# Performance work log

Hardware: AMD Instinct MI355X
Metric: run time of the kernel (lower is better)

Reference implementation:

```python
import jax, jax.numpy as jnp
import numpy as np

DELTA = 0.0          # init kwarg (torch default is 0.7; 0.0 used so random data selects pairs)
N, T = 1_048_576, 32  # samples x trait columns
COS_EPS = 1e-8       # torch.cosine_similarity eps


def setup_inputs() -> dict:
    key = jax.random.key(0)
    k1, k2 = jax.random.split(key)
    return {
        "y_pred": jax.random.normal(k1, (N, T), dtype=jnp.float32),
        "y_true": jax.random.normal(k2, (N, T), dtype=jnp.float32),
    }


def reference(y_pred, y_true):
    t = y_true.shape[1]
    # Pearson correlation matrix over columns of y_true (centered Gram + norm outer)
    xc = y_true - jnp.mean(y_true, axis=0, keepdims=True)      # [N, T]
    nx = jnp.sqrt(jnp.sum(xc * xc, axis=0))                    # [T]
    pcc = jnp.einsum('nj,nk->jk', xc, xc) / (nx[:, None] * nx[None, :])
    # Cosine similarity matrix over columns of y_pred
    pn = jnp.sqrt(jnp.sum(y_pred * y_pred, axis=0))            # [T]
    denom = jnp.maximum(pn[:, None] * pn[None, :], COS_EPS)
    cos = jnp.einsum('nj,nk->jk', y_pred, y_pred) / denom      # [T, T]
    # Pair mask: 1 <= j < k < T (loop starts at j=1 in the original)
    idx = jnp.arange(t)
    pair_mask = (idx[None, :] > idx[:, None]) & (idx[:, None] >= 1)
    sel = pair_mask & (pcc >= DELTA)
    c = (t - 1) * (t - 2) // 2                                 # total pair count (incl. unselected)
    total = jnp.sum(jnp.where(sel, 1.0 - cos, 0.0))
    return total / c
```

## Files before the change

### kernel.cpp

```cpp
#include <hip/hip_runtime.h>

#define N_ROWS   1048576
#define T_COLS   32
#define NBLK     1024
#define BLOCK    256
#define ROWS_PER_WAVEPAIR 512
#define CHUNKS   (ROWS_PER_WAVEPAIR / 16)
#define NWS      2080

typedef _Float16 half8   __attribute__((ext_vector_type(8)));
typedef float    floatx16 __attribute__((ext_vector_type(16)));

__global__ __launch_bounds__(256, 4) void ts_gram(const float* __restrict__ y_pred,
                                                  const float* __restrict__ y_true,
                                                  float* __restrict__ ws) {
    __shared__ float s_red[NWS];

    const int tid  = threadIdx.x;
    const int wv   = tid >> 6;
    const int mtx  = wv >> 1;
    const int sub  = wv & 1;
    const int lane = tid & 63;
    const int half = lane >> 5;
    const int col  = lane & 31;

    const float* src = (mtx == 0) ? y_true : y_pred;
    const size_t row0 = ((size_t)blockIdx.x * 2 + sub) * ROWS_PER_WAVEPAIR;
    const float* p = src + row0 * T_COLS + (size_t)half * 8 * T_COLS + col;

    floatx16 acc = {};
    float lsum = 0.0f;

    #pragma unroll 2
    for (int c = 0; c < CHUNKS; ++c) {
        const float* cp = p + (size_t)c * 16 * T_COLS;
        float v[8];
        #pragma unroll
        for (int j = 0; j < 8; ++j) v[j] = cp[j * T_COLS];
        half8 h;
        #pragma unroll
        for (int j = 0; j < 8; ++j) h[j] = (_Float16)v[j];
        if (mtx == 0) {
            #pragma unroll
            for (int j = 0; j < 8; ++j) lsum += v[j];
        }
        acc = __builtin_amdgcn_mfma_f32_32x32x16_f16(h, h, acc, 0, 0, 0);
    }

    for (int i = tid; i < NWS; i += BLOCK) s_red[i] = 0.0f;
    __syncthreads();
    #pragma unroll
    for (int r = 0; r < 16; ++r) {
        int row = (r & 3) + 8 * (r >> 2) + 4 * half;
        atomicAdd(&s_red[mtx * 1024 + row * 32 + col], acc[r]);
    }
    if (mtx == 0) atomicAdd(&s_red[2048 + col], lsum);
    __syncthreads();
    for (int i = tid; i < NWS; i += BLOCK) atomicAdd(&ws[i], s_red[i]);
}

__global__ __launch_bounds__(1024) void ts_final(const float* __restrict__ w,
                                                 float* __restrict__ out) {
    __shared__ float s_S[32], s_nx[32], s_pn[32];
    __shared__ float s_red[16];
    const int tid = threadIdx.x;
    const float invN = 1.0f / (float)N_ROWS;

    if (tid < 32) {
        float S = w[2048 + tid];
        s_S[tid] = S;
        float d = w[tid * 32 + tid] - S * S * invN;
        s_nx[tid] = sqrtf(d);
        s_pn[tid] = sqrtf(w[1024 + tid * 33]);
    }
    __syncthreads();

    const int j = tid >> 5, k = tid & 31;
    float contrib = 0.0f;
    if (j >= 1 && k > j) {
        float gc  = w[j * 32 + k] - s_S[j] * s_S[k] * invN;
        float pcc = gc / (s_nx[j] * s_nx[k]);
        float cs  = w[1024 + j * 32 + k] / fmaxf(s_pn[j] * s_pn[k], 1e-8f);
        if (pcc >= 0.0f) contrib = 1.0f - cs;
    }
    #pragma unroll
    for (int off = 32; off > 0; off >>= 1) contrib += __shfl_down(contrib, off);
    if ((tid & 63) == 0) s_red[tid >> 6] = contrib;
    __syncthreads();
    if (tid == 0) {
        float tot = 0.0f;
        #pragma unroll
        for (int i = 0; i < 16; ++i) tot += s_red[i];
        out[0] = tot * (1.0f / 465.0f);
    }
}

extern "C" void kernel_launch(void* const* d_in, const int* in_sizes, int n_in,
                              void* d_out, int out_size, void* d_ws, size_t ws_size,
                              hipStream_t stream) {
    const float* y_pred = (const float*)d_in[0];
    const float* y_true = (const float*)d_in[1];
    float* out = (float*)d_out;
    float* ws  = (float*)d_ws;

    hipMemsetAsync(ws, 0, NWS * sizeof(float), stream);
    ts_gram<<<NBLK, BLOCK, 0, stream>>>(y_pred, y_true, ws);
    ts_final<<<1, 1024, 0, stream>>>(ws, out);
}
```

Measured before the change: 303.7 us.

## Stage rows through LDS with vectorized loads and double-buffered prefetch

Replaces strided scalar column loads with coalesced 16-byte row loads that are converted to fp16 and written into a per-wave double-buffered LDS tile. The MFMA operands are then read back from LDS in column order. Two chunks are prefetched ahead in registers so global loads overlap the MFMA work. Blocks grow to 512 threads with four waves per matrix, and column sums use vector accumulators reduced across lanes by shuffles. The cost is extra LDS traffic and register pressure, and it relies on the LDS write and read by the same wave being ordered without a barrier.

```diff
diff --git a/kernel.cpp b/kernel.cpp
--- a/kernel.cpp
+++ b/kernel.cpp
@@ -3,58 +3,104 @@
 #define N_ROWS   1048576
 #define T_COLS   32
 #define NBLK     1024
-#define BLOCK    256
-#define ROWS_PER_WAVEPAIR 512
-#define CHUNKS   (ROWS_PER_WAVEPAIR / 16)
+#define BLOCK    512
+#define ROWS_PER_WAVE 256
+#define CH       16
 #define NWS      2080
 
-typedef _Float16 half8   __attribute__((ext_vector_type(8)));
+typedef _Float16 half8    __attribute__((ext_vector_type(8)));
+typedef _Float16 half4    __attribute__((ext_vector_type(4)));
 typedef float    floatx16 __attribute__((ext_vector_type(16)));
+typedef float    f32x4    __attribute__((ext_vector_type(4)));
 
-__global__ __launch_bounds__(256, 4) void ts_gram(const float* __restrict__ y_pred,
-                                                  const float* __restrict__ y_true,
-                                                  float* __restrict__ ws) {
-    __shared__ float s_red[NWS];
+#define LDS_ROW_H   36
+#define LDS_BUF_H   (16 * LDS_ROW_H)
+#define LDS_WAVE_H  (2 * LDS_BUF_H)
+#define LDS_BYTES   (8 * LDS_WAVE_H * 2)
+
+__global__ __launch_bounds__(BLOCK, 8) void ts_gram(const float* __restrict__ y_pred,
+                                                    const float* __restrict__ y_true,
+                                                    float* __restrict__ ws) {
+    __shared__ alignas(16) char smem[LDS_BYTES];
 
     const int tid  = threadIdx.x;
     const int wv   = tid >> 6;
-    const int mtx  = wv >> 1;
-    const int sub  = wv & 1;
+    const int mtx  = wv >> 2;
+    const int sub  = wv & 3;
     const int lane = tid & 63;
-    const int half = lane >> 5;
+    const int hi   = lane >> 5;
     const int col  = lane & 31;
+    const int lr   = lane >> 3;
+    const int lg   = lane & 7;
 
     const float* src = (mtx == 0) ? y_true : y_pred;
-    const size_t row0 = ((size_t)blockIdx.x * 2 + sub) * ROWS_PER_WAVEPAIR;
-    const float* p = src + row0 * T_COLS + (size_t)half * 8 * T_COLS + col;
+    const size_t row0 = (size_t)blockIdx.x * (4 * ROWS_PER_WAVE) + (size_t)sub * ROWS_PER_WAVE;
+    const f32x4* lp = (const f32x4*)(src + row0 * T_COLS) + lg;
+
+    _Float16* lh = (_Float16*)smem + wv * LDS_WAVE_H;
 
     floatx16 acc = {};
-    float lsum = 0.0f;
+    float cs[4] = {0.f, 0.f, 0.f, 0.f};
+    f32x4 pf[2][2];
 
-    #pragma unroll 2
-    for (int c = 0; c < CHUNKS; ++c) {
-        const float* cp = p + (size_t)c * 16 * T_COLS;
-        float v[8];
-        #pragma unroll
-        for (int j = 0; j < 8; ++j) v[j] = cp[j * T_COLS];
-        half8 h;
-        #pragma unroll
-        for (int j = 0; j < 8; ++j) h[j] = (_Float16)v[j];
-        if (mtx == 0) {
-            #pragma unroll
-            for (int j = 0; j < 8; ++j) lsum += v[j];
-        }
-        acc = __builtin_amdgcn_mfma_f32_32x32x16_f16(h, h, acc, 0, 0, 0);
+#define LOADC(c, dst) do {                                                  \
+        (dst)[0] = lp[(size_t)(((c) * 16 + 0 + lr) * 8)];                   \
+        (dst)[1] = lp[(size_t)(((c) * 16 + 8 + lr) * 8)];                   \
+    } while (0)
+
+#define STAGEC(c, s) do {                                                   \
+        _Float16* wp_ = lh + (((c) & 1) * LDS_BUF_H) + lr * LDS_ROW_H + lg * 4; \
+        _Pragma("unroll")                                                   \
+        for (int q_ = 0; q_ < 2; ++q_) {                                    \
+            f32x4 v_ = (s)[q_];                                             \
+            half4 h_;                                                       \
+            h_[0] = (_Float16)v_[0]; h_[1] = (_Float16)v_[1];               \
+            h_[2] = (_Float16)v_[2]; h_[3] = (_Float16)v_[3];               \
+            *(half4*)(wp_ + q_ * 8 * LDS_ROW_H) = h_;                       \
+            if (mtx == 0) { cs[0] += v_[0]; cs[1] += v_[1];                 \
+                            cs[2] += v_[2]; cs[3] += v_[3]; }               \
+        }                                                                   \
+    } while (0)
+
+#define COMPUTEC(c) do {                                                    \
+        const _Float16* rp_ = lh + (((c) & 1) * LDS_BUF_H) + hi * 8 * LDS_ROW_H + col; \
+        half8 h_;                                                           \
+        _Pragma("unroll")                                                   \
+        for (int j_ = 0; j_ < 8; ++j_) h_[j_] = rp_[j_ * LDS_ROW_H];        \
+        acc = __builtin_amdgcn_mfma_f32_32x32x16_f16(h_, h_, acc, 0, 0, 0); \
+    } while (0)
+
+    LOADC(0, pf[0]);
+    LOADC(1, pf[1]);
+    STAGEC(0, pf[0]);
+    #pragma unroll
+    for (int c = 0; c < CH; ++c) {
+        if (c + 2 < CH) LOADC(c + 2, pf[c & 1]);
+        if (c + 1 < CH) STAGEC(c + 1, pf[(c + 1) & 1]);
+        COMPUTEC(c);
     }
 
+    __syncthreads();
+    float* s_red = (float*)smem;
     for (int i = tid; i < NWS; i += BLOCK) s_red[i] = 0.0f;
     __syncthreads();
     #pragma unroll
     for (int r = 0; r < 16; ++r) {
-        int row = (r & 3) + 8 * (r >> 2) + 4 * half;
+        int row = (r & 3) + 8 * (r >> 2) + 4 * hi;
         atomicAdd(&s_red[mtx * 1024 + row * 32 + col], acc[r]);
     }
-    if (mtx == 0) atomicAdd(&s_red[2048 + col], lsum);
+    if (mtx == 0) {
+        #pragma unroll
+        for (int k = 0; k < 4; ++k) {
+            cs[k] += __shfl_xor(cs[k], 8);
+            cs[k] += __shfl_xor(cs[k], 16);
+            cs[k] += __shfl_xor(cs[k], 32);
+        }
+        if (lr == 0) {
+            #pragma unroll
+            for (int k = 0; k < 4; ++k) atomicAdd(&s_red[2048 + lg * 4 + k], cs[k]);
+        }
+    }
     __syncthreads();
     for (int i = tid; i < NWS; i += BLOCK) atomicAdd(&ws[i], s_red[i]);
 }
```

New measurement: 330.7 us. 8.9% more time.

## Stage Gram input through LDS with double-buffered async global_load_lds

Applied to the files above, without the earlier changes.

Each wave now streams its rows into a per-wave double buffer in LDS with global_load_lds, waiting on vmcnt so the load of chunk c+2 is in flight while chunk c is converted and fed to MFMA. Blocks grow to 512 threads with eight waves, four per matrix, each covering 256 rows. Coalesced 16-byte loads replace the strided per-column scalar loads, with the aim of hiding memory latency and improving the access pattern. The column-sum partials are combined across half-waves with a shuffle before the LDS atomic. The cost is hand-placed waitcnt and sched barriers plus extra LDS traffic.

```diff
diff --git a/kernel.cpp b/kernel.cpp
--- a/kernel.cpp
+++ b/kernel.cpp
@@ -3,58 +3,94 @@
 #define N_ROWS   1048576
 #define T_COLS   32
 #define NBLK     1024
-#define BLOCK    256
-#define ROWS_PER_WAVEPAIR 512
-#define CHUNKS   (ROWS_PER_WAVEPAIR / 16)
+#define BLOCK    512
+#define ROWS_PER_WAVE 256
+#define CH       16
 #define NWS      2080
 
-typedef _Float16 half8   __attribute__((ext_vector_type(8)));
+typedef _Float16 half8    __attribute__((ext_vector_type(8)));
 typedef float    floatx16 __attribute__((ext_vector_type(16)));
 
-__global__ __launch_bounds__(256, 4) void ts_gram(const float* __restrict__ y_pred,
-                                                  const float* __restrict__ y_true,
-                                                  float* __restrict__ ws) {
-    __shared__ float s_red[NWS];
+#define CHUNK_BYTES 2048
+#define WAVE_BYTES  (2 * CHUNK_BYTES)
+#define LDS_BYTES   (8 * WAVE_BYTES)
+
+__global__ __launch_bounds__(BLOCK, 8) void ts_gram(const float* __restrict__ y_pred,
+                                                    const float* __restrict__ y_true,
+                                                    float* __restrict__ ws) {
+    __shared__ alignas(16) char smem[LDS_BYTES];
 
     const int tid  = threadIdx.x;
     const int wv   = tid >> 6;
-    const int mtx  = wv >> 1;
-    const int sub  = wv & 1;
+    const int mtx  = wv >> 2;
+    const int sub  = wv & 3;
     const int lane = tid & 63;
-    const int half = lane >> 5;
+    const int hi   = lane >> 5;
     const int col  = lane & 31;
 
     const float* src = (mtx == 0) ? y_true : y_pred;
-    const size_t row0 = ((size_t)blockIdx.x * 2 + sub) * ROWS_PER_WAVEPAIR;
-    const float* p = src + row0 * T_COLS + (size_t)half * 8 * T_COLS + col;
+    const size_t row0 = (size_t)blockIdx.x * (4 * ROWS_PER_WAVE) + (size_t)sub * ROWS_PER_WAVE;
+    const float* gp = src + (row0 + (size_t)(lane >> 3)) * T_COLS + (lane & 7) * 4;
+
+    char* lbase = smem + wv * WAVE_BYTES;
+
+#define ISSUE(c) do {                                                         \
+        char* lb_ = lbase + (((c) & 1) * CHUNK_BYTES);                        \
+        const float* g_ = gp + (size_t)((c) * 16) * T_COLS;                   \
+        __builtin_amdgcn_global_load_lds(                                     \
+            (const __attribute__((address_space(1))) void*)g_,                \
+            (__attribute__((address_space(3))) void*)lb_, 16, 0, 0);          \
+        __builtin_amdgcn_global_load_lds(                                     \
+            (const __attribute__((address_space(1))) void*)(g_ + 8 * T_COLS), \
+            (__attribute__((address_space(3))) void*)(lb_ + 1024), 16, 0, 0); \
+    } while (0)
 
     floatx16 acc = {};
-    float lsum = 0.0f;
+    float cs = 0.0f;
 
-    #pragma unroll 2
-    for (int c = 0; c < CHUNKS; ++c) {
-        const float* cp = p + (size_t)c * 16 * T_COLS;
+    ISSUE(0);
+    ISSUE(1);
+
+    #pragma unroll
+    for (int c = 0; c < CH; ++c) {
+        if (c + 1 < CH) { asm volatile("s_waitcnt vmcnt(2)" ::: "memory"); }
+        else            { asm volatile("s_waitcnt vmcnt(0)" ::: "memory"); }
+        __builtin_amdgcn_sched_barrier(0);
+
+        const float* rp = (const float*)(lbase + (c & 1) * CHUNK_BYTES)
+                          + (size_t)hi * 8 * T_COLS + col;
         float v[8];
         #pragma unroll
-        for (int j = 0; j < 8; ++j) v[j] = cp[j * T_COLS];
+        for (int j = 0; j < 8; ++j) v[j] = rp[j * T_COLS];
+
+        asm volatile("s_waitcnt lgkmcnt(0)" ::: "memory");
+        __builtin_amdgcn_sched_barrier(0);
+        if (c + 2 < CH) ISSUE(c + 2);
+
         half8 h;
         #pragma unroll
         for (int j = 0; j < 8; ++j) h[j] = (_Float16)v[j];
         if (mtx == 0) {
             #pragma unroll
-            for (int j = 0; j < 8; ++j) lsum += v[j];
+            for (int j = 0; j < 8; ++j) cs += v[j];
         }
         acc = __builtin_amdgcn_mfma_f32_32x32x16_f16(h, h, acc, 0, 0, 0);
     }
+#undef ISSUE
 
+    __syncthreads();
+    float* s_red = (float*)smem;
     for (int i = tid; i < NWS; i += BLOCK) s_red[i] = 0.0f;
     __syncthreads();
     #pragma unroll
     for (int r = 0; r < 16; ++r) {
-        int row = (r & 3) + 8 * (r >> 2) + 4 * half;
+        int row = (r & 3) + 8 * (r >> 2) + 4 * hi;
         atomicAdd(&s_red[mtx * 1024 + row * 32 + col], acc[r]);
     }
-    if (mtx == 0) atomicAdd(&s_red[2048 + col], lsum);
+    if (mtx == 0) {
+        cs += __shfl_xor(cs, 32);
+        if (lane < 32) atomicAdd(&s_red[2048 + col], cs);
+    }
     __syncthreads();
     for (int i = tid; i < NWS; i += BLOCK) atomicAdd(&ws[i], s_red[i]);
 }
```

Result: faster. 292.7 us (-3.6%).
